# Optimization experiments

Measured on AMD Instinct MI355X. Metric: run time of the kernel, lower is better.

## Reference

```python
import jax, jax.numpy as jnp
import numpy as np

B, NQ, NK = 4, 2048, 2048
D_MODEL, H, DK, DV, M = 512, 8, 64, 64, 40


def setup_inputs() -> dict:
    key = jax.random.key(0)
    ks = jax.random.split(key, 12)
    s = 0.02  # param init scale (stand-in for xavier)
    return {
        "queries": jax.random.normal(ks[0], (B, NQ, D_MODEL), jnp.float32),
        "keys": jax.random.normal(ks[1], (B, NK, D_MODEL), jnp.float32),
        "values": jax.random.normal(ks[2], (B, NK, D_MODEL), jnp.float32),
        "attention_weights": jax.random.uniform(ks[3], (B, H, NQ, NK), jnp.float32),
        "attention_mask": jax.random.randint(ks[4], (B, H, NQ, NK), 0, 2) == 1,
        "Wq": jax.random.normal(ks[5], (D_MODEL, H * DK), jnp.float32) * s,
        "bq": jnp.zeros((H * DK,), jnp.float32),
        "Wk": jax.random.normal(ks[6], (D_MODEL, H * DK), jnp.float32) * s,
        "bk": jnp.zeros((H * DK,), jnp.float32),
        "Wv": jax.random.normal(ks[7], (D_MODEL, H * DV), jnp.float32) * s,
        "bv": jnp.zeros((H * DV,), jnp.float32),
        "Wo": jax.random.normal(ks[8], (H * DV, D_MODEL), jnp.float32) * s,
        "bo": jnp.zeros((D_MODEL,), jnp.float32),
        "m_k": jax.random.normal(ks[9], (1, M, H * DK), jnp.float32) * s,
        "m_v": jax.random.normal(ks[10], (1, M, H * DV), jnp.float32) * s,
    }


def reference(queries, keys, values, attention_weights, attention_mask,
              Wq, bq, Wk, bk, Wv, bv, Wo, bo, m_k, m_v):
    b, nq, _ = queries.shape
    nk = keys.shape[1]
    # learned memory slots, scaled and broadcast over batch
    mk = jnp.sqrt(jnp.float32(DK)) * jnp.broadcast_to(m_k, (b, M, H * DK))
    mv = jnp.sqrt(jnp.float32(M)) * jnp.broadcast_to(m_v, (b, M, H * DV))
    q = (queries @ Wq + bq).reshape(b, nq, H, DK).transpose(0, 2, 1, 3)      # (b,h,nq,dk)
    k = jnp.concatenate([keys @ Wk + bk, mk], axis=1)
    k = k.reshape(b, nk + M, H, DK).transpose(0, 2, 3, 1)                     # (b,h,dk,nk+m)
    v = jnp.concatenate([values @ Wv + bv, mv], axis=1)
    v = v.reshape(b, nk + M, H, DV).transpose(0, 2, 1, 3)                     # (b,h,nk+m,dv)
    att = jnp.matmul(q, k) / jnp.sqrt(jnp.float32(DK))                        # (b,h,nq,nk+m)
    att_x = att[..., :nk] * attention_weights
    att_x = jnp.where(attention_mask, -jnp.inf, att_x)
    att = jnp.concatenate([att_x, att[..., nk:]], axis=-1)
    att = jax.nn.softmax(att, axis=-1)
    out = jnp.matmul(att, v).transpose(0, 2, 1, 3).reshape(b, nq, H * DV)
    return out @ Wo + bo
```

## Files before the change

### kernel.cpp

```cpp
#include <hip/hip_runtime.h>
#include <hip/hip_bf16.h>
#include <cstdint>
#include <cstddef>

typedef __bf16 bf16_t;
typedef __bf16 bf16x8 __attribute__((ext_vector_type(8)));
typedef __bf16 bf16x4 __attribute__((ext_vector_type(4)));
typedef float  f32x4  __attribute__((ext_vector_type(4)));

#define B_    4
#define NQ_   2048
#define NK_   2048
#define H_    8
#define MSL_  40
#define NKP_  2112
#define SCL2  0.18033688011112042f

#define GLOAD_LDS16(GP, LP)                                                        \
    __builtin_amdgcn_global_load_lds(                                              \
        (const __attribute__((address_space(1))) unsigned int*)(GP),               \
        (__attribute__((address_space(3))) unsigned int*)(LP), 16, 0, 0)

__global__ void detect_mask(const unsigned int* __restrict__ m, int* __restrict__ flag)
{
    __shared__ int found;
    if (threadIdx.x == 0) found = 0;
    __syncthreads();
    unsigned int acc = 0;
    for (int i = threadIdx.x; i < 65536; i += 256)
        acc |= (m[i] & 0xFFFFFF00u);
    if (acc) found = 1;
    __syncthreads();
    if (threadIdx.x == 0) *flag = found;
}

__global__ void transpose_convert4(const float* __restrict__ s0, const float* __restrict__ s1,
                                   const float* __restrict__ s2, const float* __restrict__ s3,
                                   bf16_t* __restrict__ d0, bf16_t* __restrict__ d1,
                                   bf16_t* __restrict__ d2, bf16_t* __restrict__ d3)
{
    const float* src; bf16_t* dst;
    switch (blockIdx.z) {
        case 0:  src = s0; dst = d0; break;
        case 1:  src = s1; dst = d1; break;
        case 2:  src = s2; dst = d2; break;
        default: src = s3; dst = d3; break;
    }
    __shared__ float t[32][33];
    int x  = blockIdx.x * 32 + threadIdx.x;
    int y0 = blockIdx.y * 32 + threadIdx.y;
#pragma unroll
    for (int i = 0; i < 32; i += 8)
        t[threadIdx.y + i][threadIdx.x] = src[(size_t)(y0 + i) * 512 + x];
    __syncthreads();
    int ox  = blockIdx.y * 32 + threadIdx.x;
    int oy0 = blockIdx.x * 32 + threadIdx.y;
#pragma unroll
    for (int i = 0; i < 32; i += 8)
        dst[(size_t)(oy0 + i) * 512 + ox] = (bf16_t)t[threadIdx.x][threadIdx.y + i];
}

__global__ void memfill(const float* __restrict__ m_k, const float* __restrict__ m_v,
                        bf16_t* __restrict__ Kbf, bf16_t* __restrict__ Vt)
{
    int tid = blockIdx.x * 256 + threadIdx.x;
    if (tid < 4 * 64 * 512) {
        int c  = tid & 511;
        int mi = (tid >> 9) & 63;
        int b  = tid >> 15;
        float v = (mi < MSL_) ? 8.0f * m_k[mi * 512 + c] : 0.0f;
        Kbf[((size_t)b * NKP_ + NK_ + mi) * 512 + c] = (bf16_t)v;
    } else {
        int t  = tid - 4 * 64 * 512;
        int mi = t & 63;
        int dv = (t >> 6) & 63;
        int h  = (t >> 12) & 7;
        int b  = t >> 15;
        float v = (mi < MSL_) ? 6.324555320336759f * m_v[mi * 512 + h * 64 + dv] : 0.0f;
        Vt[(((size_t)b * H_ + h) * 64 + dv) * NKP_ + NK_ + mi] = (bf16_t)v;
    }
}

template<bool AF32>
__device__ __forceinline__ void gemm_core(
    bf16_t (*As)[72], bf16_t (*Bs)[72],
    const void* __restrict__ Av, const bf16_t* __restrict__ BT,
    const float* __restrict__ bias, void* __restrict__ dstv,
    int dstBS, int epi, float scale)
{
    const int tid = threadIdx.x;
    const int w = tid >> 6, l = tid & 63, lg = l >> 4, lr = l & 15;
    const int wr = w >> 1, wc = w & 1;
    const int blockM = blockIdx.x * 128, blockN = blockIdx.y * 128;

    f32x4 acc[4][4];
    const f32x4 zv = {0.f, 0.f, 0.f, 0.f};
#pragma unroll
    for (int i = 0; i < 4; i++)
#pragma unroll
        for (int j = 0; j < 4; j++) acc[i][j] = zv;

    const int ar = tid >> 1;
    const int ac = (tid & 1) * 32;

    for (int k0 = 0; k0 < 512; k0 += 64) {
        if (k0) __syncthreads();
        if constexpr (AF32) {
            const float* arow = (const float*)Av + (size_t)(blockM + ar) * 512 + k0 + ac;
#pragma unroll
            for (int i = 0; i < 8; i++) {
                float4 v = ((const float4*)arow)[i];
                bf16x4 pk = {(bf16_t)v.x, (bf16_t)v.y, (bf16_t)v.z, (bf16_t)v.w};
                *(bf16x4*)&As[ar][ac + i * 4] = pk;
            }
        } else {
            const bf16_t* arow = (const bf16_t*)Av + (size_t)(blockM + ar) * 512 + k0 + ac;
#pragma unroll
            for (int i = 0; i < 4; i++)
                *(uint4*)&As[ar][ac + i * 8] = ((const uint4*)arow)[i];
        }
        {
            const bf16_t* brow = BT + (size_t)(blockN + ar) * 512 + k0 + ac;
#pragma unroll
            for (int i = 0; i < 4; i++)
                *(uint4*)&Bs[ar][ac + i * 8] = ((const uint4*)brow)[i];
        }
        __syncthreads();
#pragma unroll
        for (int ks = 0; ks < 2; ks++) {
            bf16x8 af[4], bfr[4];
#pragma unroll
            for (int mi = 0; mi < 4; mi++)
                af[mi] = *(const bf16x8*)&As[wr * 64 + mi * 16 + lr][ks * 32 + lg * 8];
#pragma unroll
            for (int ni = 0; ni < 4; ni++)
                bfr[ni] = *(const bf16x8*)&Bs[wc * 64 + ni * 16 + lr][ks * 32 + lg * 8];
#pragma unroll
            for (int mi = 0; mi < 4; mi++)
#pragma unroll
                for (int ni = 0; ni < 4; ni++)
                    acc[mi][ni] = __builtin_amdgcn_mfma_f32_16x16x32_bf16(af[mi], bfr[ni], acc[mi][ni], 0, 0, 0);
        }
    }

    const int colbase = blockN + wc * 64;
    float bias_v[4];
#pragma unroll
    for (int ni = 0; ni < 4; ni++) bias_v[ni] = bias[colbase + ni * 16 + lr];

#pragma unroll
    for (int mi = 0; mi < 4; mi++) {
        const int r0 = blockM + wr * 64 + mi * 16 + lg * 4;
#pragma unroll
        for (int ni = 0; ni < 4; ni++) {
            const int c = colbase + ni * 16 + lr;
            f32x4 v = acc[mi][ni];
            if (epi == 2) {
                float* dst = (float*)dstv;
#pragma unroll
                for (int j = 0; j < 4; j++)
                    dst[(size_t)(r0 + j) * 512 + c] = (v[j] + bias_v[ni]) * scale;
            } else if (epi == 0) {
                bf16_t* dst = (bf16_t*)dstv;
#pragma unroll
                for (int j = 0; j < 4; j++) {
                    int rr = r0 + j;
                    int bb = rr >> 11, nn = rr & 2047;
                    dst[((size_t)bb * dstBS + nn) * 512 + c] = (bf16_t)((v[j] + bias_v[ni]) * scale);
                }
            } else {
                bf16_t* dst = (bf16_t*)dstv;
                int bb = r0 >> 11, n0 = r0 & 2047;
                int hh = c >> 6, dv = c & 63;
                bf16x4 pk;
#pragma unroll
                for (int j = 0; j < 4; j++) pk[j] = (bf16_t)((v[j] + bias_v[ni]) * scale);
                *(bf16x4*)(dst + (((size_t)bb * H_ + hh) * 64 + dv) * NKP_ + n0) = pk;
            }
        }
    }
}

__global__ __launch_bounds__(256) void gemm_qkv(
    const float* __restrict__ q, const float* __restrict__ k, const float* __restrict__ v,
    const bf16_t* __restrict__ WqT, const bf16_t* __restrict__ WkT, const bf16_t* __restrict__ WvT,
    const float* __restrict__ bq, const float* __restrict__ bk, const float* __restrict__ bv,
    bf16_t* __restrict__ Qbf, bf16_t* __restrict__ Kbf, bf16_t* __restrict__ Vt)
{
    __shared__ bf16_t As[128][72];
    __shared__ bf16_t Bs[128][72];
    const void* Av; const bf16_t* BT; const float* bias; void* dst;
    int dstBS, epi; float scale = 1.0f;
    switch (blockIdx.z) {
        case 0:  Av = q; BT = WqT; bias = bq; dst = Qbf; dstBS = 2048; epi = 0; scale = SCL2; break;
        case 1:  Av = k; BT = WkT; bias = bk; dst = Kbf; dstBS = NKP_; epi = 0; break;
        default: Av = v; BT = WvT; bias = bv; dst = Vt;  dstBS = 0;    epi = 1; break;
    }
    gemm_core<true>(As, Bs, Av, BT, bias, dst, dstBS, epi, scale);
}

__global__ __launch_bounds__(256) void gemm_fin(
    const bf16_t* __restrict__ Obuf, const bf16_t* __restrict__ WoT,
    const float* __restrict__ bo, float* __restrict__ out)
{
    __shared__ bf16_t As[128][72];
    __shared__ bf16_t Bs[128][72];
    gemm_core<false>(As, Bs, Obuf, WoT, bo, out, 0, 2, 1.0f);
}

template<bool BYTEM>
__global__ __launch_bounds__(512) void attn_fused(
    const bf16_t* __restrict__ Qbf, const bf16_t* __restrict__ Kbf,
    const bf16_t* __restrict__ Vt, const float* __restrict__ attw,
    const void* __restrict__ maskv, const int* __restrict__ mflag,
    bf16_t* __restrict__ Obuf)
{
    if ((*mflag != 0) != BYTEM) return;

    __shared__ bf16_t Ks[2][64][64];
    __shared__ bf16_t Vs[2][64][64];
    __shared__ bf16_t Pl[8][1024];

    const int tid = threadIdx.x;
    const int wv = tid >> 6, l = tid & 63, lg = l >> 4, lr = l & 15;
    const int qt = blockIdx.x, h = blockIdx.y, b = blockIdx.z;
    const int q0w = qt * 128 + wv * 16;
    bf16_t* Pw = &Pl[wv][0];

    const size_t bh = (size_t)(b * H_ + h);
    const float* wbase = attw + bh * (size_t)NQ_ * NK_;
    const unsigned char* mb8 = (const unsigned char*)maskv + bh * (size_t)NQ_ * NK_;
    const int* mb32 = (const int*)maskv + bh * (size_t)NQ_ * NK_;
    const char* kbase8 = (const char*)(Kbf + (size_t)b * NKP_ * 512 + h * 64);
    const char* vbase8 = (const char*)(Vt + bh * 64 * (size_t)NKP_);

    bf16x8 qf0 = *(const bf16x8*)&Qbf[((size_t)b * NQ_ + q0w + lr) * 512 + h * 64 + lg * 8];
    bf16x8 qf1 = *(const bf16x8*)&Qbf[((size_t)b * NQ_ + q0w + lr) * 512 + h * 64 + 32 + lg * 8];

    const f32x4 zv = {0.f, 0.f, 0.f, 0.f};
    f32x4 oacc[4];
#pragma unroll
    for (int i = 0; i < 4; i++) oacc[i] = zv;
    float mrun = -INFINITY, lsum = 0.f;
    f32x4 sA[4];

    f32x4 wA[4], wB[4];
    unsigned mA[4], mB[4];
    unsigned miA[16], miB[16];

    const int srow = l >> 3;
    const int scsw = ((l & 7) ^ (srow & 7)) * 16;

#define STAGE(BUF, KCB) do {                                                      \
    const int r_ = wv * 8 + srow;                                                 \
    GLOAD_LDS16(kbase8 + (size_t)((KCB) + r_) * 1024 + scsw,                      \
                (char*)&Ks[BUF][0][0] + wv * 1024);                               \
    GLOAD_LDS16(vbase8 + (size_t)r_ * 4224 + (size_t)(KCB) * 2 + scsw,            \
                (char*)&Vs[BUF][0][0] + wv * 1024);                               \
} while (0)

#define PREFETCH(KT, WB_, MB_, MIB_) do {                                         \
    const float* wp_ = wbase + (size_t)(q0w + lr) * NK_ + (KT) * 64 + lg * 4;     \
    _Pragma("unroll") for (int n_ = 0; n_ < 4; n_++)                              \
        WB_[n_] = *(const f32x4*)(wp_ + n_ * 16);                                 \
    if constexpr (BYTEM) {                                                        \
        const unsigned char* mp_ = mb8 + (size_t)(q0w + lr) * NK_ + (KT) * 64 + lg * 4; \
        _Pragma("unroll") for (int n_ = 0; n_ < 4; n_++)                          \
            MB_[n_] = *(const unsigned*)(mp_ + n_ * 16);                          \
    } else {                                                                      \
        const int* mp_ = mb32 + (size_t)(q0w + lr) * NK_ + (KT) * 64 + lg * 4;    \
        _Pragma("unroll") for (int n_ = 0; n_ < 4; n_++) {                        \
            uint4 t_ = *(const uint4*)(mp_ + n_ * 16);                            \
            MIB_[n_ * 4 + 0] = t_.x; MIB_[n_ * 4 + 1] = t_.y;                     \
            MIB_[n_ * 4 + 2] = t_.z; MIB_[n_ * 4 + 3] = t_.w; }                   \
    }                                                                             \
} while (0)

#define QKT_LDS(BC) do {                                                          \
    const int sw_ = (lg ^ (lr & 7)) * 8;                                          \
    _Pragma("unroll") for (int n_ = 0; n_ < 4; n_++) {                            \
        const int kr_ = n_ * 16 + lr;                                             \
        f32x4 a_ = zv;                                                            \
        a_ = __builtin_amdgcn_mfma_f32_16x16x32_bf16(*(const bf16x8*)&Ks[BC][kr_][sw_], qf0, a_, 0, 0, 0); \
        a_ = __builtin_amdgcn_mfma_f32_16x16x32_bf16(*(const bf16x8*)&Ks[BC][kr_][sw_ ^ 32], qf1, a_, 0, 0, 0); \
        sA[n_] = a_;                                                              \
    }                                                                             \
} while (0)

#define APPLY(WB_, MB_, MIB_) do {                                                \
    _Pragma("unroll") for (int n_ = 0; n_ < 4; n_++)                              \
    _Pragma("unroll") for (int j_ = 0; j_ < 4; j_++) {                            \
        bool mk_;                                                                 \
        if constexpr (BYTEM) mk_ = ((MB_[n_] >> (8 * j_)) & 0xffu) != 0;          \
        else                 mk_ = (MIB_[n_ * 4 + j_] != 0);                      \
        sA[n_][j_] = mk_ ? -1e30f : sA[n_][j_] * WB_[n_][j_];                     \
    }                                                                             \
} while (0)

#define SMPV(BC) do {                                                             \
    float tm_ = sA[0][0];                                                         \
    _Pragma("unroll") for (int n_ = 0; n_ < 4; n_++)                              \
    _Pragma("unroll") for (int j_ = 0; j_ < 4; j_++)                              \
        tm_ = fmaxf(tm_, sA[n_][j_]);                                             \
    tm_ = fmaxf(tm_, __shfl_xor(tm_, 16));                                        \
    tm_ = fmaxf(tm_, __shfl_xor(tm_, 32));                                        \
    float mnew_ = fmaxf(mrun, tm_);                                               \
    float sc_ = exp2f(mrun - mnew_);                                              \
    mrun = mnew_;                                                                 \
    float ts_ = 0.f;                                                              \
    _Pragma("unroll") for (int n_ = 0; n_ < 4; n_++)                              \
    _Pragma("unroll") for (int j_ = 0; j_ < 4; j_++) {                            \
        float p_ = exp2f(sA[n_][j_] - mnew_);                                     \
        sA[n_][j_] = p_; ts_ += p_;                                               \
    }                                                                             \
    ts_ += __shfl_xor(ts_, 16);                                                   \
    ts_ += __shfl_xor(ts_, 32);                                                   \
    lsum = lsum * sc_ + ts_;                                                      \
    _Pragma("unroll") for (int n2_ = 0; n2_ < 4; n2_++) oacc[n2_] *= sc_;         \
    _Pragma("unroll") for (int n_ = 0; n_ < 4; n_++) {                            \
        int c_ = n_ * 2 + (lg >> 1);                                              \
        int qp_ = (lr + 4 * c_) & 15;                                             \
        bf16x4 pk_ = {(bf16_t)sA[n_][0], (bf16_t)sA[n_][1],                       \
                      (bf16_t)sA[n_][2], (bf16_t)sA[n_][3]};                      \
        *(bf16x4*)&Pw[c_ * 128 + qp_ * 8 + (lg & 1) * 4] = pk_;                   \
    }                                                                             \
    bf16x8 pf0_ = *(const bf16x8*)&Pw[lg * 128 + ((lr + 4 * lg) & 15) * 8];       \
    bf16x8 pf1_ = *(const bf16x8*)&Pw[(4 + lg) * 128 + ((lr + 4 * (4 + lg)) & 15) * 8]; \
    const int vsw_ = (lg ^ (lr & 7)) * 8;                                         \
    _Pragma("unroll") for (int n2_ = 0; n2_ < 4; n2_++) {                         \
        const int vr_ = n2_ * 16 + lr;                                            \
        oacc[n2_] = __builtin_amdgcn_mfma_f32_16x16x32_bf16(*(const bf16x8*)&Vs[BC][vr_][vsw_], pf0_, oacc[n2_], 0, 0, 0); \
        oacc[n2_] = __builtin_amdgcn_mfma_f32_16x16x32_bf16(*(const bf16x8*)&Vs[BC][vr_][vsw_ ^ 32], pf1_, oacc[n2_], 0, 0, 0); \
    }                                                                             \
} while (0)

#define WAITBAR(WCNT) do {                                                        \
    asm volatile("s_waitcnt vmcnt(" WCNT ")" ::: "memory");                       \
    __builtin_amdgcn_s_barrier();                                                 \
    __builtin_amdgcn_sched_barrier(0);                                            \
} while (0)

#define BODY(KT, BC, BN, WC_, MC_, MIC_) do {                                     \
    WAITBAR("8");                                                                 \
    if ((KT) < 31) { STAGE(BN, ((KT) + 1) * 64); }                                \
    __builtin_amdgcn_sched_barrier(0);                                            \
    QKT_LDS(BC);                                                                  \
    APPLY(WC_, MC_, MIC_);                                                        \
    if ((KT) < 30) { PREFETCH((KT) + 2, WC_, MC_, MIC_); }                        \
    SMPV(BC);                                                                     \
} while (0)

    STAGE(0, 2048);
    __builtin_amdgcn_sched_barrier(0);
    PREFETCH(0, wA, mA, miA);

    {
        WAITBAR("8");
        STAGE(1, 0);
        __builtin_amdgcn_sched_barrier(0);
        QKT_LDS(0);
#pragma unroll
        for (int n_ = 0; n_ < 4; n_++)
#pragma unroll
            for (int j_ = 0; j_ < 4; j_++) {
                int kloc = n_ * 16 + lg * 4 + j_;
                sA[n_][j_] = (kloc >= MSL_) ? -1e30f : sA[n_][j_];
            }
        PREFETCH(1, wB, mB, miB);
        SMPV(0);
    }

    for (int kt = 0; kt < 30; kt += 2) {
        BODY(kt,     1, 0, wA, mA, miA);
        BODY(kt + 1, 0, 1, wB, mB, miB);
    }
    BODY(30, 1, 0, wA, mA, miA);
    {
        WAITBAR("0");
        QKT_LDS(0);
        APPLY(wB, mB, miB);
        SMPV(0);
    }

    float invl = 1.0f / lsum;
#pragma unroll
    for (int n2 = 0; n2 < 4; n2++) {
        bf16x4 ov = {(bf16_t)(oacc[n2][0] * invl), (bf16_t)(oacc[n2][1] * invl),
                     (bf16_t)(oacc[n2][2] * invl), (bf16_t)(oacc[n2][3] * invl)};
        *(bf16x4*)&Obuf[((size_t)b * NQ_ + q0w + lr) * 512 + h * 64 + n2 * 16 + lg * 4] = ov;
    }

#undef STAGE
#undef PREFETCH
#undef QKT_LDS
#undef APPLY
#undef SMPV
#undef WAITBAR
#undef BODY
}

extern "C" void kernel_launch(void* const* d_in, const int* in_sizes, int n_in,
                              void* d_out, int out_size, void* d_ws, size_t ws_size,
                              hipStream_t stream)
{
    const float* queries = (const float*)d_in[0];
    const float* keys    = (const float*)d_in[1];
    const float* values  = (const float*)d_in[2];
    const float* attw    = (const float*)d_in[3];
    const void*  maskv   = d_in[4];
    const float* Wq = (const float*)d_in[5];
    const float* bq = (const float*)d_in[6];
    const float* Wk = (const float*)d_in[7];
    const float* bk = (const float*)d_in[8];
    const float* Wv = (const float*)d_in[9];
    const float* bv = (const float*)d_in[10];
    const float* Wo = (const float*)d_in[11];
    const float* bo = (const float*)d_in[12];
    const float* m_k = (const float*)d_in[13];
    const float* m_v = (const float*)d_in[14];

    char* ws = (char*)d_ws;
    bf16_t* WqT  = (bf16_t*)(ws + 0);
    bf16_t* WkT  = (bf16_t*)(ws + 524288);
    bf16_t* WvT  = (bf16_t*)(ws + 1048576);
    bf16_t* WoT  = (bf16_t*)(ws + 1572864);
    bf16_t* Qbf  = (bf16_t*)(ws + 2097152);
    bf16_t* Kbf  = (bf16_t*)(ws + 10485760);
    bf16_t* Vt   = (bf16_t*)(ws + 19136512);
    bf16_t* Obuf = (bf16_t*)(ws + 27787264);
    int*    mflag = (int*)(ws + 36175872);

    detect_mask<<<1, 256, 0, stream>>>((const unsigned int*)maskv, mflag);
    transpose_convert4<<<dim3(16, 16, 4), dim3(32, 8), 0, stream>>>(
        Wq, Wk, Wv, Wo, WqT, WkT, WvT, WoT);
    memfill<<<1024, 256, 0, stream>>>(m_k, m_v, Kbf, Vt);

    gemm_qkv<<<dim3(64, 4, 3), 256, 0, stream>>>(
        queries, keys, values, WqT, WkT, WvT, bq, bk, bv, Qbf, Kbf, Vt);

    attn_fused<true><<<dim3(16, H_, B_), 512, 0, stream>>>(Qbf, Kbf, Vt, attw, maskv, mflag, Obuf);
    attn_fused<false><<<dim3(16, H_, B_), 512, 0, stream>>>(Qbf, Kbf, Vt, attw, maskv, mflag, Obuf);

    gemm_fin<<<dim3(64, 4), 256, 0, stream>>>(Obuf, WoT, bo, (float*)d_out);
    (void)in_sizes; (void)n_in; (void)out_size; (void)ws_size;
}
```

Before: 344.0 us.

## Split attention over key halves with flash-decoding style merge kernel

Restructures the fused attention kernel to split the key dimension into two halves per (batch, head, query tile), using smaller 256-thread blocks with 64-query tiles and 32-key steps, so the grid has many more blocks. Each half writes fp32 partial outputs plus running max and sum, and a new merge kernel combines them into the bf16 output. The goal is more parallelism and occupancy for the memory-bound stream of attention weights and mask. In exchange it adds fp32 partial traffic, an extra launch, and a simpler __syncthreads double-buffer pipeline in place of the tuned vmcnt-based one.

```diff
diff --git a/kernel.cpp b/kernel.cpp
--- a/kernel.cpp
+++ b/kernel.cpp
@@ -209,25 +209,27 @@
 }
 
 template<bool BYTEM>
-__global__ __launch_bounds__(512) void attn_fused(
+__global__ __launch_bounds__(256) void attn_ks(
     const bf16_t* __restrict__ Qbf, const bf16_t* __restrict__ Kbf,
     const bf16_t* __restrict__ Vt, const float* __restrict__ attw,
     const void* __restrict__ maskv, const int* __restrict__ mflag,
-    bf16_t* __restrict__ Obuf)
+    float* __restrict__ Opart, float* __restrict__ mlbuf)
 {
     if ((*mflag != 0) != BYTEM) return;
 
-    __shared__ bf16_t Ks[2][64][64];
-    __shared__ bf16_t Vs[2][64][64];
-    __shared__ bf16_t Pl[8][1024];
+    __shared__ bf16_t Ks[2][32][64];
+    __shared__ bf16_t Vs[2][64][32];
+    __shared__ bf16_t Pl[4][512];
 
     const int tid = threadIdx.x;
     const int wv = tid >> 6, l = tid & 63, lg = l >> 4, lr = l & 15;
-    const int qt = blockIdx.x, h = blockIdx.y, b = blockIdx.z;
-    const int q0w = qt * 128 + wv * 16;
+    const int qt = blockIdx.x, h = blockIdx.y;
+    const int b = blockIdx.z >> 1, ks = blockIdx.z & 1;
+    const int q0w = qt * 64 + wv * 16;
     bf16_t* Pw = &Pl[wv][0];
 
     const size_t bh = (size_t)(b * H_ + h);
+    const int kb = ks * 1024;
     const float* wbase = attw + bh * (size_t)NQ_ * NK_;
     const unsigned char* mb8 = (const unsigned char*)maskv + bh * (size_t)NQ_ * NK_;
     const int* mb32 = (const int*)maskv + bh * (size_t)NQ_ * NK_;
@@ -242,43 +244,42 @@
 #pragma unroll
     for (int i = 0; i < 4; i++) oacc[i] = zv;
     float mrun = -INFINITY, lsum = 0.f;
-    f32x4 sA[4];
-
-    f32x4 wA[4], wB[4];
-    unsigned mA[4], mB[4];
-    unsigned miA[16], miB[16];
-
-    const int srow = l >> 3;
-    const int scsw = ((l & 7) ^ (srow & 7)) * 16;
-
-#define STAGE(BUF, KCB) do {                                                      \
-    const int r_ = wv * 8 + srow;                                                 \
-    GLOAD_LDS16(kbase8 + (size_t)((KCB) + r_) * 1024 + scsw,                      \
+    f32x4 sA[2];
+    f32x4 wA[2];
+    unsigned mA[2];
+    unsigned miA[8];
+
+    const int ksrow = l >> 3;
+    const int kss = (((l & 7) ^ (ksrow & 7)) * 16);
+    const int vss = ((((l & 3) ^ ((l >> 3) & 3))) * 16);
+
+#define STAGE32(BUF, KRB) do {                                                    \
+    GLOAD_LDS16(kbase8 + (size_t)((KRB) + wv * 8 + ksrow) * 1024 + kss,           \
                 (char*)&Ks[BUF][0][0] + wv * 1024);                               \
-    GLOAD_LDS16(vbase8 + (size_t)r_ * 4224 + (size_t)(KCB) * 2 + scsw,            \
+    GLOAD_LDS16(vbase8 + (size_t)(wv * 16 + (l >> 2)) * 4224 + (size_t)(KRB) * 2 + vss, \
                 (char*)&Vs[BUF][0][0] + wv * 1024);                               \
 } while (0)
 
-#define PREFETCH(KT, WB_, MB_, MIB_) do {                                         \
-    const float* wp_ = wbase + (size_t)(q0w + lr) * NK_ + (KT) * 64 + lg * 4;     \
-    _Pragma("unroll") for (int n_ = 0; n_ < 4; n_++)                              \
-        WB_[n_] = *(const f32x4*)(wp_ + n_ * 16);                                 \
+#define PREFETCH32(KCOL) do {                                                     \
+    const float* wp_ = wbase + (size_t)(q0w + lr) * NK_ + (KCOL) + lg * 4;        \
+    wA[0] = *(const f32x4*)(wp_);                                                 \
+    wA[1] = *(const f32x4*)(wp_ + 16);                                            \
     if constexpr (BYTEM) {                                                        \
-        const unsigned char* mp_ = mb8 + (size_t)(q0w + lr) * NK_ + (KT) * 64 + lg * 4; \
-        _Pragma("unroll") for (int n_ = 0; n_ < 4; n_++)                          \
-            MB_[n_] = *(const unsigned*)(mp_ + n_ * 16);                          \
+        const unsigned char* mp_ = mb8 + (size_t)(q0w + lr) * NK_ + (KCOL) + lg * 4; \
+        mA[0] = *(const unsigned*)(mp_);                                          \
+        mA[1] = *(const unsigned*)(mp_ + 16);                                     \
     } else {                                                                      \
-        const int* mp_ = mb32 + (size_t)(q0w + lr) * NK_ + (KT) * 64 + lg * 4;    \
-        _Pragma("unroll") for (int n_ = 0; n_ < 4; n_++) {                        \
-            uint4 t_ = *(const uint4*)(mp_ + n_ * 16);                            \
-            MIB_[n_ * 4 + 0] = t_.x; MIB_[n_ * 4 + 1] = t_.y;                     \
-            MIB_[n_ * 4 + 2] = t_.z; MIB_[n_ * 4 + 3] = t_.w; }                   \
+        const int* mp_ = mb32 + (size_t)(q0w + lr) * NK_ + (KCOL) + lg * 4;       \
+        uint4 t0_ = *(const uint4*)(mp_);                                         \
+        uint4 t1_ = *(const uint4*)(mp_ + 16);                                    \
+        miA[0]=t0_.x; miA[1]=t0_.y; miA[2]=t0_.z; miA[3]=t0_.w;                   \
+        miA[4]=t1_.x; miA[5]=t1_.y; miA[6]=t1_.z; miA[7]=t1_.w;                   \
     }                                                                             \
 } while (0)
 
-#define QKT_LDS(BC) do {                                                          \
+#define QKT32(BC) do {                                                            \
     const int sw_ = (lg ^ (lr & 7)) * 8;                                          \
-    _Pragma("unroll") for (int n_ = 0; n_ < 4; n_++) {                            \
+    _Pragma("unroll") for (int n_ = 0; n_ < 2; n_++) {                            \
         const int kr_ = n_ * 16 + lr;                                             \
         f32x4 a_ = zv;                                                            \
         a_ = __builtin_amdgcn_mfma_f32_16x16x32_bf16(*(const bf16x8*)&Ks[BC][kr_][sw_], qf0, a_, 0, 0, 0); \
@@ -287,19 +288,19 @@
     }                                                                             \
 } while (0)
 
-#define APPLY(WB_, MB_, MIB_) do {                                                \
-    _Pragma("unroll") for (int n_ = 0; n_ < 4; n_++)                              \
+#define APPLY32() do {                                                            \
+    _Pragma("unroll") for (int n_ = 0; n_ < 2; n_++)                              \
     _Pragma("unroll") for (int j_ = 0; j_ < 4; j_++) {                            \
         bool mk_;                                                                 \
-        if constexpr (BYTEM) mk_ = ((MB_[n_] >> (8 * j_)) & 0xffu) != 0;          \
-        else                 mk_ = (MIB_[n_ * 4 + j_] != 0);                      \
-        sA[n_][j_] = mk_ ? -1e30f : sA[n_][j_] * WB_[n_][j_];                     \
+        if constexpr (BYTEM) mk_ = ((mA[n_] >> (8 * j_)) & 0xffu) != 0;           \
+        else                 mk_ = (miA[n_ * 4 + j_] != 0);                       \
+        sA[n_][j_] = mk_ ? -1e30f : sA[n_][j_] * wA[n_][j_];                      \
     }                                                                             \
 } while (0)
 
-#define SMPV(BC) do {                                                             \
+#define SMPV32(BC) do {                                                           \
     float tm_ = sA[0][0];                                                         \
-    _Pragma("unroll") for (int n_ = 0; n_ < 4; n_++)                              \
+    _Pragma("unroll") for (int n_ = 0; n_ < 2; n_++)                              \
     _Pragma("unroll") for (int j_ = 0; j_ < 4; j_++)                              \
         tm_ = fmaxf(tm_, sA[n_][j_]);                                             \
     tm_ = fmaxf(tm_, __shfl_xor(tm_, 16));                                        \
@@ -308,7 +309,7 @@
     float sc_ = exp2f(mrun - mnew_);                                              \
     mrun = mnew_;                                                                 \
     float ts_ = 0.f;                                                              \
-    _Pragma("unroll") for (int n_ = 0; n_ < 4; n_++)                              \
+    _Pragma("unroll") for (int n_ = 0; n_ < 2; n_++)                              \
     _Pragma("unroll") for (int j_ = 0; j_ < 4; j_++) {                            \
         float p_ = exp2f(sA[n_][j_] - mnew_);                                     \
         sA[n_][j_] = p_; ts_ += p_;                                               \
@@ -317,7 +318,7 @@
     ts_ += __shfl_xor(ts_, 32);                                                   \
     lsum = lsum * sc_ + ts_;                                                      \
     _Pragma("unroll") for (int n2_ = 0; n2_ < 4; n2_++) oacc[n2_] *= sc_;         \
-    _Pragma("unroll") for (int n_ = 0; n_ < 4; n_++) {                            \
+    _Pragma("unroll") for (int n_ = 0; n_ < 2; n_++) {                            \
         int c_ = n_ * 2 + (lg >> 1);                                              \
         int qp_ = (lr + 4 * c_) & 15;                                             \
         bf16x4 pk_ = {(bf16_t)sA[n_][0], (bf16_t)sA[n_][1],                       \
@@ -325,78 +326,93 @@
         *(bf16x4*)&Pw[c_ * 128 + qp_ * 8 + (lg & 1) * 4] = pk_;                   \
     }                                                                             \
     bf16x8 pf0_ = *(const bf16x8*)&Pw[lg * 128 + ((lr + 4 * lg) & 15) * 8];       \
-    bf16x8 pf1_ = *(const bf16x8*)&Pw[(4 + lg) * 128 + ((lr + 4 * (4 + lg)) & 15) * 8]; \
-    const int vsw_ = (lg ^ (lr & 7)) * 8;                                         \
+    const int vsw_ = (lg ^ ((lr >> 1) & 3)) * 8;                                  \
     _Pragma("unroll") for (int n2_ = 0; n2_ < 4; n2_++) {                         \
         const int vr_ = n2_ * 16 + lr;                                            \
         oacc[n2_] = __builtin_amdgcn_mfma_f32_16x16x32_bf16(*(const bf16x8*)&Vs[BC][vr_][vsw_], pf0_, oacc[n2_], 0, 0, 0); \
-        oacc[n2_] = __builtin_amdgcn_mfma_f32_16x16x32_bf16(*(const bf16x8*)&Vs[BC][vr_][vsw_ ^ 32], pf1_, oacc[n2_], 0, 0, 0); \
     }                                                                             \
 } while (0)
 
-#define WAITBAR(WCNT) do {                                                        \
-    asm volatile("s_waitcnt vmcnt(" WCNT ")" ::: "memory");                       \
-    __builtin_amdgcn_s_barrier();                                                 \
-    __builtin_amdgcn_sched_barrier(0);                                            \
-} while (0)
-
-#define BODY(KT, BC, BN, WC_, MC_, MIC_) do {                                     \
-    WAITBAR("8");                                                                 \
-    if ((KT) < 31) { STAGE(BN, ((KT) + 1) * 64); }                                \
-    __builtin_amdgcn_sched_barrier(0);                                            \
-    QKT_LDS(BC);                                                                  \
-    APPLY(WC_, MC_, MIC_);                                                        \
-    if ((KT) < 30) { PREFETCH((KT) + 2, WC_, MC_, MIC_); }                        \
-    SMPV(BC);                                                                     \
-} while (0)
-
-    STAGE(0, 2048);
-    __builtin_amdgcn_sched_barrier(0);
-    PREFETCH(0, wA, mA, miA);
-
-    {
-        WAITBAR("8");
-        STAGE(1, 0);
-        __builtin_amdgcn_sched_barrier(0);
-        QKT_LDS(0);
-#pragma unroll
-        for (int n_ = 0; n_ < 4; n_++)
+    if (ks) {
+        STAGE32(0, 2048);
+        STAGE32(1, 2080);
+        PREFETCH32(1024);
+        __syncthreads();
+        QKT32(0);
+#pragma unroll
+        for (int n_ = 0; n_ < 2; n_++)
 #pragma unroll
             for (int j_ = 0; j_ < 4; j_++) {
                 int kloc = n_ * 16 + lg * 4 + j_;
                 sA[n_][j_] = (kloc >= MSL_) ? -1e30f : sA[n_][j_];
             }
-        PREFETCH(1, wB, mB, miB);
-        SMPV(0);
-    }
-
-    for (int kt = 0; kt < 30; kt += 2) {
-        BODY(kt,     1, 0, wA, mA, miA);
-        BODY(kt + 1, 0, 1, wB, mB, miB);
-    }
-    BODY(30, 1, 0, wA, mA, miA);
+        SMPV32(0);
+        __syncthreads();
+        STAGE32(0, 1024);
+        QKT32(1);
+#pragma unroll
+        for (int n_ = 0; n_ < 2; n_++)
+#pragma unroll
+            for (int j_ = 0; j_ < 4; j_++) {
+                int kloc = 32 + n_ * 16 + lg * 4 + j_;
+                sA[n_][j_] = (kloc >= MSL_) ? -1e30f : sA[n_][j_];
+            }
+        SMPV32(1);
+        __syncthreads();
+    } else {
+        STAGE32(0, 0);
+        PREFETCH32(0);
+        __syncthreads();
+    }
+
+    int cur = 0;
+    for (int t = 0; t < 32; ++t) {
+        if (t < 31) STAGE32(cur ^ 1, kb + (t + 1) * 32);
+        QKT32(cur);
+        APPLY32();
+        if (t < 31) PREFETCH32(kb + (t + 1) * 32);
+        SMPV32(cur);
+        __syncthreads();
+        cur ^= 1;
+    }
+
     {
-        WAITBAR("0");
-        QKT_LDS(0);
-        APPLY(wB, mB, miB);
-        SMPV(0);
-    }
-
-    float invl = 1.0f / lsum;
-#pragma unroll
-    for (int n2 = 0; n2 < 4; n2++) {
-        bf16x4 ov = {(bf16_t)(oacc[n2][0] * invl), (bf16_t)(oacc[n2][1] * invl),
-                     (bf16_t)(oacc[n2][2] * invl), (bf16_t)(oacc[n2][3] * invl)};
-        *(bf16x4*)&Obuf[((size_t)b * NQ_ + q0w + lr) * 512 + h * 64 + n2 * 16 + lg * 4] = ov;
-    }
-
-#undef STAGE
-#undef PREFETCH
-#undef QKT_LDS
-#undef APPLY
-#undef SMPV
-#undef WAITBAR
-#undef BODY
+        float* op = Opart + (((size_t)(bh * 2 + ks)) * 2048 + q0w + lr) * 64;
+#pragma unroll
+        for (int n2 = 0; n2 < 4; n2++)
+            *(f32x4*)(op + n2 * 16 + lg * 4) = oacc[n2];
+        if (l < 16) {
+            float2 v = make_float2(mrun, lsum);
+            *(float2*)&mlbuf[((bh * 2 + ks) * 2048 + q0w + l) * 2] = v;
+        }
+    }
+
+#undef STAGE32
+#undef PREFETCH32
+#undef QKT32
+#undef APPLY32
+#undef SMPV32
+}
+
+__global__ __launch_bounds__(256) void merge_ks(
+    const float* __restrict__ Opart, const float* __restrict__ mlbuf,
+    bf16_t* __restrict__ Obuf)
+{
+    int tid = blockIdx.x * 256 + threadIdx.x;
+    int c4  = tid & 15;
+    int bhq = tid >> 4;
+    int bh = bhq >> 11, q = bhq & 2047;
+    float2 a = *(const float2*)&mlbuf[((bh * 2 + 0) * 2048 + q) * 2];
+    float2 c = *(const float2*)&mlbuf[((bh * 2 + 1) * 2048 + q) * 2];
+    float m  = fmaxf(a.x, c.x);
+    float s0 = exp2f(a.x - m), s1 = exp2f(c.x - m);
+    float inv = 1.0f / (a.y * s0 + c.y * s1);
+    f32x4 o0 = *(const f32x4*)&Opart[(((size_t)(bh * 2 + 0)) * 2048 + q) * 64 + c4 * 4];
+    f32x4 o1 = *(const f32x4*)&Opart[(((size_t)(bh * 2 + 1)) * 2048 + q) * 64 + c4 * 4];
+    bf16x4 r;
+#pragma unroll
+    for (int j = 0; j < 4; j++) r[j] = (bf16_t)((o0[j] * s0 + o1[j] * s1) * inv);
+    *(bf16x4*)&Obuf[((size_t)(bh >> 3) * 2048 + q) * 512 + (bh & 7) * 64 + c4 * 4] = r;
 }
 
 extern "C" void kernel_launch(void* const* d_in, const int* in_sizes, int n_in,
@@ -429,6 +445,8 @@
     bf16_t* Vt   = (bf16_t*)(ws + 19136512);
     bf16_t* Obuf = (bf16_t*)(ws + 27787264);
     int*    mflag = (int*)(ws + 36175872);
+    float*  Opart = (float*)(ws + 36176896);
+    float*  mlbuf = (float*)(ws + 69731328);
 
     detect_mask<<<1, 256, 0, stream>>>((const unsigned int*)maskv, mflag);
     transpose_convert4<<<dim3(16, 16, 4), dim3(32, 8), 0, stream>>>(
@@ -438,8 +456,9 @@
     gemm_qkv<<<dim3(64, 4, 3), 256, 0, stream>>>(
         queries, keys, values, WqT, WkT, WvT, bq, bk, bv, Qbf, Kbf, Vt);
 
-    attn_fused<true><<<dim3(16, H_, B_), 512, 0, stream>>>(Qbf, Kbf, Vt, attw, maskv, mflag, Obuf);
-    attn_fused<false><<<dim3(16, H_, B_), 512, 0, stream>>>(Qbf, Kbf, Vt, attw, maskv, mflag, Obuf);
+    attn_ks<true><<<dim3(32, H_, 8), 256, 0, stream>>>(Qbf, Kbf, Vt, attw, maskv, mflag, Opart, mlbuf);
+    attn_ks<false><<<dim3(32, H_, 8), 256, 0, stream>>>(Qbf, Kbf, Vt, attw, maskv, mflag, Opart, mlbuf);
+    merge_ks<<<4096, 256, 0, stream>>>(Opart, mlbuf, Obuf);
 
     gemm_fin<<<dim3(64, 4), 256, 0, stream>>>(Obuf, WoT, bo, (float*)d_out);
     (void)in_sizes; (void)n_in; (void)out_size; (void)ws_size;
```

After: 400.0 us. 16.3% more time.
